# Kernel optimization log

Hardware: AMD Instinct MI355X
Metric: run time of the kernel (lower is better)

The kernel has to match this reference:

```python
import jax, jax.numpy as jnp
import numpy as np

B, T, C = 2, 2048, 2048
N_HEAD = 16
HD = C // N_HEAD  # 128


def setup_inputs() -> dict:
    key = jax.random.key(0)
    k1, k2, k3, k4, k5 = jax.random.split(key, 5)
    s_in = 1.0 / np.sqrt(C)
    return {
        "x": jax.random.normal(k1, (B, T, C), dtype=jnp.float32),
        # weights stored as (in, out), i.e. transpose of torch Linear weight
        "W_attn": jax.random.normal(k2, (C, 3 * C), dtype=jnp.float32) * s_in,
        "b_attn": jax.random.normal(k3, (3 * C,), dtype=jnp.float32) * 0.02,
        "W_proj": jax.random.normal(k4, (C, C), dtype=jnp.float32) * s_in,
        "b_proj": jax.random.normal(k5, (C,), dtype=jnp.float32) * 0.02,
    }


def reference(x, W_attn, b_attn, W_proj, b_proj):
    # qkv projection: (B,T,3C)
    qkv = x @ W_attn + b_attn
    q, k, v = jnp.split(qkv, 3, axis=-1)
    # (B, n_head, T, head_dim)
    q = q.reshape(B, T, N_HEAD, HD).transpose(0, 2, 1, 3)
    k = k.reshape(B, T, N_HEAD, HD).transpose(0, 2, 1, 3)
    v = v.reshape(B, T, N_HEAD, HD).transpose(0, 2, 1, 3)
    # scores (B,H,T,T), causal mask (T_q == T_k prefill path)
    att = jnp.einsum("bhqd,bhkd->bhqk", q, k) * (1.0 / np.sqrt(HD))
    causal = jnp.tril(jnp.ones((T, T), dtype=bool))
    att = jnp.where(causal[None, None], att, -jnp.inf)
    att = jax.nn.softmax(att, axis=-1)  # attn_dropout is identity (p=0)
    y = jnp.einsum("bhqk,bhkd->bhqd", att, v)
    y = y.transpose(0, 2, 1, 3).reshape(B, T, C)
    y = y @ W_proj + b_proj  # resid_dropout identity (p=0)
    # new_cache = (k, v, T) since T == block_size; return output tensor
    return y
```

## Files before the change

kernel.cpp:

```cpp
#include <hip/hip_runtime.h>
#include <cstdint>
#include <cstddef>


typedef __bf16 bf16x8 __attribute__((ext_vector_type(8)));
typedef float  f32x4  __attribute__((ext_vector_type(4)));
typedef unsigned short u16x4 __attribute__((ext_vector_type(4)));
typedef unsigned short u16x8 __attribute__((ext_vector_type(8)));

__device__ __forceinline__ unsigned short f2bf(float f) {
  unsigned int u = __builtin_bit_cast(unsigned int, f);
  u += 0x7fffu + ((u >> 16) & 1u);
  return (unsigned short)(u >> 16);
}

__device__ __forceinline__ void gld16(void* lds, const void* g) {
  __builtin_amdgcn_global_load_lds(
      (const __attribute__((address_space(1))) void*)g,
      (__attribute__((address_space(3))) void*)lds, 16, 0, 0);
}

__global__ void cvt_f32_bf16_k(const float* __restrict__ in,
                               unsigned short* __restrict__ out, int n4) {
  int i = blockIdx.x * blockDim.x + threadIdx.x;
  int stride = gridDim.x * blockDim.x;
  for (; i < n4; i += stride) {
    float4 v = ((const float4*)in)[i];
    ushort4 o;
    o.x = f2bf(v.x); o.y = f2bf(v.y); o.z = f2bf(v.z); o.w = f2bf(v.w);
    ((ushort4*)out)[i] = o;
  }
}

__global__ __launch_bounds__(256) void transpose_f32_bf16(
    const float* __restrict__ in, unsigned short* __restrict__ out,
    int R, int C) {
  __shared__ float tile[64][65];
  int c0 = blockIdx.x * 64, r0 = blockIdx.y * 64;
  int t = threadIdx.x;
  int lr = t >> 4, lc = (t & 15) * 4;
#pragma unroll
  for (int i = 0; i < 4; i++) {
    int row = lr + i * 16;
    float4 v = *(const float4*)&in[(size_t)(r0 + row) * C + c0 + lc];
    tile[row][lc] = v.x; tile[row][lc + 1] = v.y;
    tile[row][lc + 2] = v.z; tile[row][lc + 3] = v.w;
  }
  __syncthreads();
  int wr = t >> 3, wc = (t & 7) * 8;
#pragma unroll
  for (int i = 0; i < 2; i++) {
    int crow = wr + i * 32;
    u16x8 o;
#pragma unroll
    for (int j = 0; j < 8; j++) o[j] = f2bf(tile[wc + j][crow]);
    *(u16x8*)&out[(size_t)(c0 + crow) * R + r0 + wc] = o;
  }
}

__global__ __launch_bounds__(256) void extract_vT_k(
    const unsigned short* __restrict__ qkv, unsigned short* __restrict__ vT) {
  __shared__ unsigned int tile32[64][33];
  int bh = blockIdx.z, b = bh >> 4, h = bh & 15;
  int t0 = blockIdx.x * 64, d0 = blockIdx.y * 64;
  int t = threadIdx.x;
  int lr = t >> 3, lc = (t & 7) * 8;
  const unsigned short* src = qkv + (size_t)(b * 2048) * 6144 + 4096 + h * 128;
#pragma unroll
  for (int i = 0; i < 2; i++) {
    int row = lr + i * 32;
    u16x8 v = *(const u16x8*)&src[(size_t)(t0 + row) * 6144 + d0 + lc];
#pragma unroll
    for (int j = 0; j < 8; j++) {
      unsigned short* p = (unsigned short*)&tile32[lc + j][row & 31];
      p[row >> 5] = v[j];
    }
  }
  __syncthreads();
  int dr = t >> 2, tc = (t & 3) * 8;
  u16x8 lo, hi;
#pragma unroll
  for (int j = 0; j < 8; j++) {
    unsigned int u = tile32[dr][tc + j];
    lo[j] = (unsigned short)(u & 0xffffu);
    hi[j] = (unsigned short)(u >> 16);
  }
  unsigned short* dst = vT + (size_t)bh * 128 * 2048 + (size_t)(d0 + dr) * 2048 + t0;
  *(u16x8*)&dst[tc] = lo;
  *(u16x8*)&dst[tc + 32] = hi;
}

template <int OUT_BF16>
__global__ __launch_bounds__(256) void gemm_bt(
    const unsigned short* __restrict__ A, const unsigned short* __restrict__ BT,
    const float* __restrict__ bias, void* __restrict__ Cout,
    int M, int N, int K) {
  __shared__ __align__(16) unsigned short sA[128 * 64];
  __shared__ __align__(16) unsigned short sB[128 * 64];

  const int tid = threadIdx.x, w = tid >> 6, lane = tid & 63;
  const int quad = lane >> 4, l16 = lane & 15;
  const int m0 = blockIdx.y * 128, n0 = blockIdx.x * 128;
  const int wr = w >> 1, wc = w & 1;

  const unsigned short* gA[4];
  const unsigned short* gB[4];
  unsigned short* lA[4];
  unsigned short* lB[4];
#pragma unroll
  for (int i = 0; i < 4; i++) {
    int c = w * 256 + i * 64 + lane;
    int row = c >> 3, scol = (c & 7) ^ (row & 7);
    gA[i] = A + (size_t)(m0 + row) * K + scol * 8;
    gB[i] = BT + (size_t)(n0 + row) * K + scol * 8;
    lA[i] = sA + (size_t)(w * 256 + i * 64) * 8;
    lB[i] = sB + (size_t)(w * 256 + i * 64) * 8;
  }

  f32x4 acc[4][4] = {};

  for (int k0 = 0; k0 < K; k0 += 64) {
#pragma unroll
    for (int i = 0; i < 4; i++) {
      gld16(lA[i], gA[i]); gld16(lB[i], gB[i]);
      gA[i] += 64; gB[i] += 64;
    }
    __syncthreads();

#pragma unroll
    for (int kk = 0; kk < 2; kk++) {
      const int cc = (kk * 4 + quad) ^ (l16 & 7);
      bf16x8 af[4], bfr[4];
#pragma unroll
      for (int mi = 0; mi < 4; mi++)
        af[mi] = *(const bf16x8*)&sA[(wr * 64 + mi * 16 + l16) * 64 + cc * 8];
#pragma unroll
      for (int ni = 0; ni < 4; ni++)
        bfr[ni] = *(const bf16x8*)&sB[(wc * 64 + ni * 16 + l16) * 64 + cc * 8];
#pragma unroll
      for (int mi = 0; mi < 4; mi++)
#pragma unroll
        for (int ni = 0; ni < 4; ni++)
          acc[mi][ni] = __builtin_amdgcn_mfma_f32_16x16x32_bf16(
              af[mi], bfr[ni], acc[mi][ni], 0, 0, 0);
    }
    __syncthreads();
  }

#pragma unroll
  for (int mi = 0; mi < 4; mi++) {
    int row = m0 + wr * 64 + mi * 16 + quad * 4;
#pragma unroll
    for (int ni = 0; ni < 4; ni++) {
      int col = n0 + wc * 64 + ni * 16 + l16;
      float bv = bias[col];
#pragma unroll
      for (int r = 0; r < 4; r++) {
        float v = acc[mi][ni][r] + bv;
        if (OUT_BF16)
          ((unsigned short*)Cout)[(size_t)(row + r) * N + col] = f2bf(v);
        else
          ((float*)Cout)[(size_t)(row + r) * N + col] = v;
      }
    }
  }
}

#define BARRIER8 __builtin_amdgcn_s_barrier()
#define WAIT_LGKM0 asm volatile("s_waitcnt lgkmcnt(0)" ::: "memory")
#define WAIT_VM2 asm volatile("s_waitcnt vmcnt(2)" ::: "memory")
#define WAIT_VM0 asm volatile("s_waitcnt vmcnt(0)" ::: "memory")

#define STAGE_A(buf, h, t)                                                   \
  do {                                                                       \
    gld16(&sA[buf][((h) * 1024 + w * 64) * 8],                               \
          gA0 + (size_t)(h) * 128 * K + (size_t)(t) * 64);                   \
    gld16(&sA[buf][((h) * 1024 + 512 + w * 64) * 8],                         \
          gA1 + (size_t)(h) * 128 * K + (size_t)(t) * 64);                   \
  } while (0)

#define STAGE_B(buf, h, t)                                                   \
  do {                                                                       \
    gld16(&sB[buf][((h) * 1024 + w * 64) * 8],                               \
          gB0 + (size_t)(h) * 128 * K + (size_t)(t) * 64);                   \
    gld16(&sB[buf][((h) * 1024 + 512 + w * 64) * 8],                         \
          gB1 + (size_t)(h) * 128 * K + (size_t)(t) * 64);                   \
  } while (0)

#define LDA4(buf, mh, kk)                                                    \
  do {                                                                       \
    const int cc_ = ((kk) * 4 + quad) ^ (l16 & 7);                           \
    _Pragma("unroll") for (int i_ = 0; i_ < 4; ++i_) {                       \
      const int rr_ = wr * 128 + (mh) * 64 + i_ * 16 + l16;                  \
      a_[i_] = *(const bf16x8*)&sA[buf][rr_ * 64 + cc_ * 8];                 \
    }                                                                        \
  } while (0)

#define LDB4(buf, kk)                                                        \
  do {                                                                       \
    const int cc_ = ((kk) * 4 + quad) ^ (l16 & 7);                           \
    _Pragma("unroll") for (int i_ = 0; i_ < 4; ++i_) {                       \
      const int rr_ = wc * 64 + i_ * 16 + l16;                               \
      b_[i_] = *(const bf16x8*)&sB[buf][rr_ * 64 + cc_ * 8];                 \
    }                                                                        \
  } while (0)

#define MM16(mh)                                                             \
  do {                                                                       \
    __builtin_amdgcn_s_setprio(1);                                           \
    _Pragma("unroll") for (int i_ = 0; i_ < 4; ++i_)                         \
    _Pragma("unroll") for (int n_ = 0; n_ < 4; ++n_)                         \
        acc[(mh) * 4 + i_][n_] = __builtin_amdgcn_mfma_f32_16x16x32_bf16(    \
            a_[i_], b_[n_], acc[(mh) * 4 + i_][n_], 0, 0, 0);                \
    __builtin_amdgcn_s_setprio(0);                                           \
  } while (0)

template <int OUT_BF16>
__global__ __launch_bounds__(512, 2) void gemm_bt8(
    const unsigned short* __restrict__ A, const unsigned short* __restrict__ BT,
    const float* __restrict__ bias, void* __restrict__ Cout,
    int M, int N, int K) {
  __shared__ __align__(16) unsigned short sA[2][256 * 64];
  __shared__ __align__(16) unsigned short sB[2][256 * 64];
  (void)M;

  const int tid = threadIdx.x, w = tid >> 6, lane = tid & 63;
  const int quad = lane >> 4, l16 = lane & 15;
  const int wr = w >> 2, wc = w & 3;

  const int nwgx = gridDim.x;
  const int nwg = nwgx * gridDim.y;
  const int wg = blockIdx.y * nwgx + blockIdx.x;
  const int q8 = nwg >> 3, r8 = nwg & 7;
  const int xcd = wg & 7, loc = wg >> 3;
  const int swz =
      (xcd < r8 ? xcd * (q8 + 1) : r8 * (q8 + 1) + (xcd - r8) * q8) + loc;
  const int m0 = (swz / nwgx) * 256;
  const int n0 = (swz % nwgx) * 256;

  const int c0 = tid, c1 = tid + 512;
  const int r0c = c0 >> 3, s0c = (c0 & 7) ^ (r0c & 7);
  const int r1c = c1 >> 3, s1c = (c1 & 7) ^ (r1c & 7);
  const unsigned short* gA0 = A + (size_t)(m0 + r0c) * K + s0c * 8;
  const unsigned short* gA1 = A + (size_t)(m0 + r1c) * K + s1c * 8;
  const unsigned short* gB0 = BT + (size_t)(n0 + r0c) * K + s0c * 8;
  const unsigned short* gB1 = BT + (size_t)(n0 + r1c) * K + s1c * 8;

  f32x4 acc[8][4] = {};
  bf16x8 a_[4], b_[4];

  const int NT = K >> 6;
  const int NI = NT >> 1;

  STAGE_B(0, 0, 0); STAGE_B(0, 1, 0);
  STAGE_A(0, 0, 0); STAGE_A(0, 1, 0);
  STAGE_B(1, 0, 1);
  WAIT_VM2;
  BARRIER8;

  for (int i = 0; i < NI; ++i) {
    const int t1 = 2 * i + 1;
    const int tn0 = 2 * i + 2, tn1 = 2 * i + 3;
    const bool last = (i == NI - 1);

    LDB4(0, 0); LDA4(0, 0, 0);
    STAGE_B(1, 1, t1);
    BARRIER8; WAIT_LGKM0; MM16(0); BARRIER8;

    LDA4(0, 1, 0);
    STAGE_A(1, 0, t1);
    BARRIER8; WAIT_LGKM0; MM16(1); BARRIER8;

    LDB4(0, 1); LDA4(0, 0, 1);
    STAGE_A(1, 1, t1);
    BARRIER8; WAIT_LGKM0; MM16(0); BARRIER8;

    LDA4(0, 1, 1);
    if (!last) STAGE_B(0, 0, tn0);
    if (last) { WAIT_VM0; } else { WAIT_VM2; }
    BARRIER8; WAIT_LGKM0; MM16(1); BARRIER8;

    LDB4(1, 0); LDA4(1, 0, 0);
    if (!last) STAGE_B(0, 1, tn0);
    BARRIER8; WAIT_LGKM0; MM16(0); BARRIER8;

    LDA4(1, 1, 0);
    if (!last) STAGE_A(0, 0, tn0);
    BARRIER8; WAIT_LGKM0; MM16(1); BARRIER8;

    LDB4(1, 1); LDA4(1, 0, 1);
    if (!last) STAGE_A(0, 1, tn0);
    BARRIER8; WAIT_LGKM0; MM16(0); BARRIER8;

    LDA4(1, 1, 1);
    if (!last) STAGE_B(1, 0, tn1);
    if (!last) { WAIT_VM2; }
    BARRIER8; WAIT_LGKM0; MM16(1); BARRIER8;
  }

#pragma unroll
  for (int mi = 0; mi < 8; ++mi) {
    int row = m0 + wr * 128 + mi * 16 + quad * 4;
#pragma unroll
    for (int ni = 0; ni < 4; ++ni) {
      int col = n0 + wc * 64 + ni * 16 + l16;
      float bv = bias[col];
#pragma unroll
      for (int rr = 0; rr < 4; ++rr) {
        float v = acc[mi][ni][rr] + bv;
        if (OUT_BF16)
          ((unsigned short*)Cout)[(size_t)(row + rr) * N + col] = f2bf(v);
        else
          ((float*)Cout)[(size_t)(row + rr) * N + col] = v;
      }
    }
  }
}

#undef STAGE_A
#undef STAGE_B
#undef LDA4
#undef LDB4
#undef MM16

__global__ __launch_bounds__(256) void flash_attn(
    const unsigned short* __restrict__ qkv, const unsigned short* __restrict__ vT,
    unsigned short* __restrict__ yout) {
  __shared__ __align__(16) unsigned short sK[2][64 * 128];
  __shared__ __align__(16) unsigned short sVT[2][128 * 64];
  __shared__ __align__(16) unsigned short sP[4 * 16 * 64];

  const int tid = threadIdx.x, w = tid >> 6, lane = tid & 63;
  const int quad = lane >> 4, l16 = lane & 15;
  const int id = blockIdx.x;
  const int g = id & 31;
  const int qp = id >> 5;
  const int b = g >> 4, h = g & 15;
  const int T = 2048, CC = 6144, HD = 128;
  const float qscale = 0.12753257252f;

  const unsigned short* gK = qkv + (size_t)(b * T) * CC + 2048 + h * HD;
  const unsigned short* gV = vT + (size_t)(b * 16 + h) * HD * T;
  unsigned short* pw = sP + w * 16 * 64;

  const unsigned short* kSrc[4];
  const unsigned short* vSrc[4];
  unsigned short* kDst[4];
  unsigned short* vDst[4];
#pragma unroll
  for (int i = 0; i < 4; i++) {
    int c = w * 256 + i * 64 + lane;
    int kR = c >> 4, kC = (c & 15) ^ (kR & 15);
    int vR = c >> 3, vC = (c & 7) ^ (vR & 7);
    kSrc[i] = gK + (size_t)kR * CC + kC * 8;
    vSrc[i] = gV + (size_t)vR * T + vC * 8;
    kDst[i] = (unsigned short*)sK + (size_t)(w * 256 + i * 64) * 8;
    vDst[i] = (unsigned short*)sVT + (size_t)(w * 256 + i * 64) * 8;
  }
  const int KBUF = 64 * 128, VBUF = 128 * 64;

  const int qtA = qp, qtB = 31 - qp;
  int qt = qtA, kt = 0;

  bf16x8 qf[4];
  float m_old, l_sum;
  f32x4 o[8] = {};
  {
    const size_t qrow = (size_t)(b * T + qt * 64 + w * 16 + l16) * CC + h * HD;
#pragma unroll
    for (int kb = 0; kb < 4; kb++) {
      bf16x8 raw = *(const bf16x8*)&qkv[qrow + kb * 32 + quad * 8];
      bf16x8 sc;
#pragma unroll
      for (int j = 0; j < 8; j++) sc[j] = (__bf16)((float)raw[j] * qscale);
      qf[kb] = sc;
    }
  }
  m_old = -1e30f; l_sum = 0.f;

#pragma unroll
  for (int i = 0; i < 4; i++) {
    gld16(kDst[i], kSrc[i]);
    gld16(vDst[i], vSrc[i]);
  }

  const int total = qtA + qtB + 2;
  for (int it = 0; it < total; ++it) {
    __syncthreads();
    const int cur = it & 1;
    const bool segEnd = (kt == qt);

    if (it + 1 < total) {
      const int nkt = segEnd ? 0 : kt + 1;
      const int nb_ = (it + 1) & 1;
      const size_t kOff = (size_t)nkt * 64 * CC;
      const int vOff = nkt * 64;
#pragma unroll
      for (int i = 0; i < 4; i++) {
        gld16(kDst[i] + (size_t)nb_ * KBUF, kSrc[i] + kOff);
        gld16(vDst[i] + (size_t)nb_ * VBUF, vSrc[i] + vOff);
      }
    }

    const unsigned short* sKc = (const unsigned short*)sK + (size_t)cur * KBUF;
    const unsigned short* sVc = (const unsigned short*)sVT + (size_t)cur * VBUF;

    f32x4 s4[4] = {};
#pragma unroll
    for (int dc = 0; dc < 4; dc++) {
#pragma unroll
      for (int kb = 0; kb < 4; kb++) {
        int rr = kb * 16 + l16;
        int cc = (dc * 4 + quad) ^ l16;
        bf16x8 kf = *(const bf16x8*)&sKc[rr * 128 + cc * 8];
        s4[kb] = __builtin_amdgcn_mfma_f32_16x16x32_bf16(kf, qf[dc], s4[kb], 0, 0, 0);
      }
    }

    float sv[4][4];
#pragma unroll
    for (int kb = 0; kb < 4; kb++)
#pragma unroll
      for (int r = 0; r < 4; r++) {
        float v = s4[kb][r];
        if (segEnd) {
          if (kb * 16 + quad * 4 + r > w * 16 + l16) v = -1e30f;
        }
        sv[kb][r] = v;
      }

    float mx = sv[0][0];
#pragma unroll
    for (int kb = 0; kb < 4; kb++)
#pragma unroll
      for (int r = 0; r < 4; r++) mx = fmaxf(mx, sv[kb][r]);
    mx = fmaxf(mx, __shfl_xor(mx, 16));
    mx = fmaxf(mx, __shfl_xor(mx, 32));
    float m_new = fmaxf(m_old, mx);
    float a = exp2f(m_old - m_new);
    float ssum = 0.f;
#pragma unroll
    for (int kb = 0; kb < 4; kb++)
#pragma unroll
      for (int r = 0; r < 4; r++) {
        float p = exp2f(sv[kb][r] - m_new);
        sv[kb][r] = p;
        ssum += p;
      }
    ssum += __shfl_xor(ssum, 16);
    ssum += __shfl_xor(ssum, 32);
    l_sum = l_sum * a + ssum;
    m_old = m_new;

    float ar[4];
#pragma unroll
    for (int r = 0; r < 4; r++)
      ar[r] = __shfl(a, (lane & 48) + quad * 4 + r);
#pragma unroll
    for (int nb = 0; nb < 8; nb++)
#pragma unroll
      for (int r = 0; r < 4; r++) o[nb][r] *= ar[r];

#pragma unroll
    for (int kb = 0; kb < 4; kb++) {
      u16x4 pk;
#pragma unroll
      for (int r = 0; r < 4; r++) pk[r] = f2bf(sv[kb][r]);
      int c = kb * 2 + (quad >> 1);
      int cp = c ^ (l16 & 7);
      *(u16x4*)&pw[l16 * 64 + cp * 8 + (quad & 1) * 4] = pk;
    }

#pragma unroll
    for (int kb2 = 0; kb2 < 2; kb2++) {
      int pcc = (kb2 * 4 + quad) ^ (l16 & 7);
      bf16x8 pf = *(const bf16x8*)&pw[l16 * 64 + pcc * 8];
#pragma unroll
      for (int nb = 0; nb < 8; nb++) {
        int rr = nb * 16 + l16;
        int cc = (kb2 * 4 + quad) ^ (rr & 7);
        bf16x8 vf = *(const bf16x8*)&sVc[rr * 64 + cc * 8];
        o[nb] = __builtin_amdgcn_mfma_f32_16x16x32_bf16(pf, vf, o[nb], 0, 0, 0);
      }
    }

    if (segEnd) {
      float linv = 1.0f / l_sum;
#pragma unroll
      for (int r = 0; r < 4; r++) {
        float ir = __shfl(linv, (lane & 48) + quad * 4 + r);
        size_t orow = (size_t)(b * T + qt * 64 + w * 16 + quad * 4 + r) * 2048 + h * HD;
#pragma unroll
        for (int nb = 0; nb < 8; nb++)
          yout[orow + nb * 16 + l16] = f2bf(o[nb][r] * ir);
      }
      if (it + 1 < total) {
        qt = qtB;
        const size_t qrow = (size_t)(b * T + qt * 64 + w * 16 + l16) * CC + h * HD;
#pragma unroll
        for (int kb = 0; kb < 4; kb++) {
          bf16x8 raw = *(const bf16x8*)&qkv[qrow + kb * 32 + quad * 8];
          bf16x8 sc;
#pragma unroll
          for (int j = 0; j < 8; j++) sc[j] = (__bf16)((float)raw[j] * qscale);
          qf[kb] = sc;
        }
        m_old = -1e30f; l_sum = 0.f;
#pragma unroll
        for (int nb = 0; nb < 8; nb++) o[nb] = (f32x4){0.f, 0.f, 0.f, 0.f};
      }
      kt = 0;
    } else {
      kt++;
    }
  }
}

extern "C" void kernel_launch(void* const* d_in, const int* in_sizes, int n_in,
                              void* d_out, int out_size, void* d_ws, size_t ws_size,
                              hipStream_t stream) {
  const float* x      = (const float*)d_in[0];
  const float* W_attn = (const float*)d_in[1];
  const float* b_attn = (const float*)d_in[2];
  const float* W_proj = (const float*)d_in[3];
  const float* b_proj = (const float*)d_in[4];
  float* out = (float*)d_out;

  char* ws = (char*)d_ws;
  unsigned short* x_bf  = (unsigned short*)(ws);
  unsigned short* WaT   = (unsigned short*)(ws + 16777216);
  unsigned short* WpT   = (unsigned short*)(ws + 41943040);
  unsigned short* qkv   = (unsigned short*)(ws + 50331648);
  unsigned short* vT    = (unsigned short*)(ws + 100663296);
  unsigned short* y_att = (unsigned short*)(ws + 117440512);

  cvt_f32_bf16_k<<<1024, 256, 0, stream>>>(x, x_bf, 8388608 / 4);
  transpose_f32_bf16<<<dim3(96, 32), 256, 0, stream>>>(W_attn, WaT, 2048, 6144);
  transpose_f32_bf16<<<dim3(32, 32), 256, 0, stream>>>(W_proj, WpT, 2048, 2048);
  gemm_bt8<1><<<dim3(24, 16), 512, 0, stream>>>(x_bf, WaT, b_attn, qkv, 4096, 6144, 2048);
  extract_vT_k<<<dim3(32, 2, 32), 256, 0, stream>>>(qkv, vT);
  flash_attn<<<dim3(512), 256, 0, stream>>>(qkv, vT, y_att);
  gemm_bt<0><<<dim3(16, 32), 256, 0, stream>>>(y_att, WpT, b_proj, out, 4096, 2048, 2048);
}
```

Before: 422.9 us.

## Remap A-tile row ownership and prefetch A/B halves together in 256x256 GEMM

Changes which rows of the A tile each wave reads, so each M-half of the LDS tile corresponds to one staged half. A and B halves for the same K tile are then staged together, with deeper vmcnt waits (4 instead of 2). The intent is to issue global-to-LDS loads earlier and in larger batches, so memory latency overlaps better with the MFMA phases. The epilogue row mapping is updated to match, and the change adds more outstanding loads and relies on the new wait counts being correct for LDS buffer reuse.

```diff
diff --git a/kernel.cpp b/kernel.cpp
--- a/kernel.cpp
+++ b/kernel.cpp
@@ -168,7 +168,7 @@
 
 #define BARRIER8 __builtin_amdgcn_s_barrier()
 #define WAIT_LGKM0 asm volatile("s_waitcnt lgkmcnt(0)" ::: "memory")
-#define WAIT_VM2 asm volatile("s_waitcnt vmcnt(2)" ::: "memory")
+#define WAIT_VM4 asm volatile("s_waitcnt vmcnt(4)" ::: "memory")
 #define WAIT_VM0 asm volatile("s_waitcnt vmcnt(0)" ::: "memory")
 
 #define STAGE_A(buf, h, t)                                                   \
@@ -191,7 +191,7 @@
   do {                                                                       \
     const int cc_ = ((kk) * 4 + quad) ^ (l16 & 7);                           \
     _Pragma("unroll") for (int i_ = 0; i_ < 4; ++i_) {                       \
-      const int rr_ = wr * 128 + (mh) * 64 + i_ * 16 + l16;                  \
+      const int rr_ = (mh) * 128 + wr * 64 + i_ * 16 + l16;                  \
       a_[i_] = *(const bf16x8*)&sA[buf][rr_ * 64 + cc_ * 8];                 \
     }                                                                        \
   } while (0)
@@ -252,10 +252,10 @@
   const int NT = K >> 6;
   const int NI = NT >> 1;
 
-  STAGE_B(0, 0, 0); STAGE_B(0, 1, 0);
-  STAGE_A(0, 0, 0); STAGE_A(0, 1, 0);
-  STAGE_B(1, 0, 1);
-  WAIT_VM2;
+  STAGE_B(0, 0, 0); STAGE_A(0, 0, 0);
+  STAGE_B(0, 1, 0); STAGE_A(0, 1, 0);
+  STAGE_B(1, 0, 1); STAGE_A(1, 0, 1);
+  WAIT_VM4;
   BARRIER8;
 
   for (int i = 0; i < NI; ++i) {
@@ -264,43 +264,46 @@
     const bool last = (i == NI - 1);
 
     LDB4(0, 0); LDA4(0, 0, 0);
-    STAGE_B(1, 1, t1);
+    STAGE_B(1, 1, t1); STAGE_A(1, 1, t1);
     BARRIER8; WAIT_LGKM0; MM16(0); BARRIER8;
 
     LDA4(0, 1, 0);
-    STAGE_A(1, 0, t1);
     BARRIER8; WAIT_LGKM0; MM16(1); BARRIER8;
 
     LDB4(0, 1); LDA4(0, 0, 1);
-    STAGE_A(1, 1, t1);
     BARRIER8; WAIT_LGKM0; MM16(0); BARRIER8;
 
     LDA4(0, 1, 1);
-    if (!last) STAGE_B(0, 0, tn0);
-    if (last) { WAIT_VM0; } else { WAIT_VM2; }
+    if (!last) {
+      STAGE_B(0, 0, tn0); STAGE_A(0, 0, tn0);
+      WAIT_VM4;
+    } else {
+      WAIT_VM0;
+    }
     BARRIER8; WAIT_LGKM0; MM16(1); BARRIER8;
 
     LDB4(1, 0); LDA4(1, 0, 0);
-    if (!last) STAGE_B(0, 1, tn0);
+    if (!last) { STAGE_B(0, 1, tn0); STAGE_A(0, 1, tn0); }
     BARRIER8; WAIT_LGKM0; MM16(0); BARRIER8;
 
     LDA4(1, 1, 0);
-    if (!last) STAGE_A(0, 0, tn0);
     BARRIER8; WAIT_LGKM0; MM16(1); BARRIER8;
 
     LDB4(1, 1); LDA4(1, 0, 1);
-    if (!last) STAGE_A(0, 1, tn0);
     BARRIER8; WAIT_LGKM0; MM16(0); BARRIER8;
 
     LDA4(1, 1, 1);
-    if (!last) STAGE_B(1, 0, tn1);
-    if (!last) { WAIT_VM2; }
+    if (!last) {
+      STAGE_B(1, 0, tn1); STAGE_A(1, 0, tn1);
+      WAIT_VM4;
+    }
     BARRIER8; WAIT_LGKM0; MM16(1); BARRIER8;
   }
 
 #pragma unroll
   for (int mi = 0; mi < 8; ++mi) {
-    int row = m0 + wr * 128 + mi * 16 + quad * 4;
+    const int mh = mi >> 2, i2 = mi & 3;
+    int row = m0 + mh * 128 + wr * 64 + i2 * 16 + quad * 4;
 #pragma unroll
     for (int ni = 0; ni < 4; ++ni) {
       int col = n0 + wc * 64 + ni * 16 + l16;
```

After: 402.2 us. 4.9% less time.
